# Kernel optimization log

Hardware: AMD Instinct MI355X
Metric: run time of the kernel (lower is better)

The kernel has to match this reference:

```python
import jax, jax.numpy as jnp
import numpy as np

WS = 8  # window size (8,8); num_token n = 64


def setup_inputs() -> dict:
    key = jax.random.key(0)
    ks = jax.random.split(key, 10)
    dim = 28        # channels c
    d = 28          # dim_head
    rank = 28       # sq_dim
    n = WS * WS     # tokens per window
    x = jax.random.normal(ks[0], (1, 8, 256, 256, dim), jnp.float32)

    def lin(k, shape, fan_in):
        return jax.random.normal(k, shape, jnp.float32) / np.sqrt(fan_in).astype(np.float32)

    return {
        "x": x,
        "W_qk": lin(ks[1], (2 * rank, dim), dim),   # to_qk (no bias)
        "W_v": lin(ks[2], (dim, dim), dim),         # to_v (no bias)
        "W_out": lin(ks[3], (dim, dim), dim),       # to_out weight
        "b_out": jnp.zeros((dim,), jnp.float32),    # to_out bias
        "W_pcq": lin(ks[4], (1, d), d),             # pc_proj_q
        "b_pcq": jnp.ones((1,), jnp.float32),       # bias_pc_proj_q (init 1.0)
        "W_pck": lin(ks[5], (1, d), d),             # pc_proj_k
        "b_pck": jnp.ones((1,), jnp.float32),
        "W_m1": lin(ks[6], (1, n), n),              # mlp1: Linear(64,1)
        "W_m2a": lin(ks[7], (n, n), n),             # mlp2: Linear(64,64)
        "W_m2b": lin(ks[8], (1, n), n),             # mlp2: Linear(64,1)
    }


def _fa_forward(x, W_qk, W_v, W_out, b_out, W_pcq, b_pcq, W_pck, b_pck, W_m1, W_m2a, W_m2b):
    b, B, H, Wd, c = x.shape
    nh, nw = H // WS, Wd // WS
    n = WS * WS
    heads = 1  # dim_head == dim == sq_dim -> heads_qk = heads_v = 1
    # window partition: 'b B (h b0) (w b1) c -> (b h w) (b0 b1) B c'
    xw = (x.reshape(b, B, nh, WS, nw, WS, c)
           .transpose(0, 2, 4, 3, 5, 1, 6)
           .reshape(b * nh * nw, n, B, c))
    qk = xw @ W_qk.T                      # [w, n, B, 2*rank]
    q, k = jnp.split(qk, 2, axis=-1)
    v = xw @ W_v.T

    def split_heads(t):                   # [w, n, B, h*d] -> [w, h, B, n, d]
        w_, n_, B_, _ = t.shape
        return t.reshape(w_, n_, B_, heads, -1).transpose(0, 3, 2, 1, 4)

    q, k, v = split_heads(q), split_heads(k), split_heads(v)

    # learned sigma per token
    sig_q = q @ W_pcq.T + b_pcq           # [w, h, B, n, 1]
    sig_k = k @ W_pck.T + b_pck
    sim = jnp.einsum('whBid,whBjd->whBij', q, k)          # raw scores
    Sigma = sig_q * jnp.swapaxes(sig_k, -1, -2)           # outer product [.., i, j]
    # diagonal removal: sim - diag_embed(diag(sim)) == zero the diagonal
    eye = jnp.eye(n, dtype=sim.dtype)
    sim_norm = sim * (1.0 - eye)
    # MLP threshold
    theta = jnp.einsum('whBij,j->whBi', sim_norm, W_m1[0])  # mlp1 over j, squeeze
    t = theta @ W_m2a.T
    t = jnp.where(t >= 0, t, 0.1 * t)                       # LeakyReLU(0.1)
    theta = (t @ W_m2b.T)[..., None]                        # [w, h, B, 1, 1]
    sim = sim * Sigma
    attn = jax.nn.softmax(sim, axis=-1) * (sim > theta).astype(sim.dtype)
    out = jnp.einsum('whBij,whBjd->whBid', attn, v)
    # merge heads: [w, h, B, n, d] -> [w, n, B, h*d]
    out = out.transpose(0, 3, 2, 1, 4).reshape(b * nh * nw, n, B, c)
    out = out @ W_out.T + b_out
    # un-window: '(b h w) (b0 b1) B c -> b B (h b0) (w b1) c'
    out = (out.reshape(b, nh, nw, WS, WS, B, c)
              .transpose(0, 5, 1, 3, 2, 4, 6)
              .reshape(b, B, H, Wd, c))
    return out


def reference(x, W_qk, W_v, W_out, b_out, W_pcq, b_pcq, W_pck, b_pck, W_m1, W_m2a, W_m2b):
    return _fa_forward(x, W_qk, W_v, W_out, b_out, W_pcq, b_pcq,
                       W_pck, b_pck, W_m1, W_m2a, W_m2b)
```

## Files before the change

kernel.cpp:

```cpp
#include <hip/hip_runtime.h>
#include <math.h>

#define C 28
#define N 64

typedef float ff2 __attribute__((ext_vector_type(2)));

#define A_OFF   0
#define QT_OFF  0
#define KT_OFF  1792
#define V_OFF   2048
#define SQ_OFF  3840
#define SGK_OFF 3904
#define TH_OFF  3968
#define LDS_FLOATS 4032

__device__ __forceinline__ float prefix8_asc(float s) {
    float p = s;
    #pragma unroll
    for (int k = 0; k < 7; ++k) {
        int sh = __builtin_amdgcn_update_dpp(0, __float_as_int(p),
                                             0x111 , 0xF, 0xF, true);
        p = __int_as_float(sh) + s;
    }
    return p;
}

__device__ __forceinline__ float max8_dpp(float m) {
    int t;
    t = __builtin_amdgcn_update_dpp(0, __float_as_int(m), 0xB1,  0xF, 0xF, true);
    m = fmaxf(m, __int_as_float(t));
    t = __builtin_amdgcn_update_dpp(0, __float_as_int(m), 0x4E,  0xF, 0xF, true);
    m = fmaxf(m, __int_as_float(t));
    t = __builtin_amdgcn_update_dpp(0, __float_as_int(m), 0x141, 0xF, 0xF, true);
    m = fmaxf(m, __int_as_float(t));
    return m;
}

__global__ __launch_bounds__(128, 8)
void fa_tiled(const float* __restrict__ x,
              const float* __restrict__ Wqk,
              const float* __restrict__ Wv,
              const float* __restrict__ Wout,
              const float* __restrict__ bout,
              const float* __restrict__ Wpcq,
              const float* __restrict__ bpcq,
              const float* __restrict__ Wpck,
              const float* __restrict__ bpck,
              const float* __restrict__ Wm1,
              const float* __restrict__ Wm2a,
              const float* __restrict__ Wm2b,
              float* __restrict__ out)
{
    __shared__ float S[LDS_FLOATS];

    const int tid = threadIdx.x;
    const int wv  = tid >> 6;
    const int ln  = tid & 63;
    const int pid = blockIdx.x;
    const int win = pid >> 3;
    const int Bi  = pid & 7;
    const int hw = win >> 5, ww = win & 31;
    const int b0 = ln >> 3, b1 = ln & 7;
    const size_t base = ((((size_t)Bi * 256) + (size_t)(hw * 8 + b0)) * 256
                         + (size_t)(ww * 8 + b1)) * C;

    const int ti = tid >> 3;
    const int tj = tid & 7;
    const int rg = ti & 7;
    const int gb = ln & 56;

    float vv[16];

    {
        float xr[C];
        {
            const float4* p = (const float4*)(x + base);
            #pragma unroll
            for (int i = 0; i < 7; ++i) {
                float4 t = p[i];
                xr[4*i+0] = t.x; xr[4*i+1] = t.y; xr[4*i+2] = t.z; xr[4*i+3] = t.w;
            }
        }

        if (wv == 0) {
            ff2 sq2 = {0.f, 0.f};
            #pragma unroll 2
            for (int d4 = 0; d4 < 7; ++d4) {
                float qq[4];
                #pragma unroll
                for (int t = 0; t < 4; ++t) {
                    const int d = 4*d4 + t;
                    ff2 a = {0.f, 0.f};
                    #pragma unroll
                    for (int c = 0; c < C; c += 2) {
                        ff2 w = *(const ff2*)&Wqk[d*C + c];
                        ff2 xv; xv.x = xr[c]; xv.y = xr[c+1];
                        a += w * xv;
                    }
                    qq[t] = a.x + a.y;
                    S[QT_OFF + d*64 + ln] = qq[t];
                }
                ff2 q01; q01.x = qq[0]; q01.y = qq[1];
                ff2 q23; q23.x = qq[2]; q23.y = qq[3];
                ff2 w01 = *(const ff2*)&Wpcq[4*d4];
                ff2 w23 = *(const ff2*)&Wpcq[4*d4+2];
                sq2 += q01 * w01;
                sq2 += q23 * w23;
            }
            S[SQ_OFF + ln] = sq2.x + sq2.y + bpcq[0];
            #pragma unroll
            for (int d4 = 0; d4 < 4; ++d4) {
                #pragma unroll
                for (int t = 0; t < 4; ++t) {
                    const int d = 4*d4 + t;
                    ff2 a = {0.f, 0.f};
                    #pragma unroll
                    for (int c = 0; c < C; c += 2) {
                        ff2 w = *(const ff2*)&Wv[d*C + c];
                        ff2 xv; xv.x = xr[c]; xv.y = xr[c+1];
                        a += w * xv;
                    }
                    vv[4*d4+t] = a.x + a.y;
                }
            }
        } else {
            float ak = 0.f;
            #pragma unroll 2
            for (int d4 = 0; d4 < 7; ++d4) {
                float kk[4];
                #pragma unroll
                for (int t = 0; t < 4; ++t) {
                    const int d = 4*d4 + t;
                    ff2 a = {0.f, 0.f};
                    #pragma unroll
                    for (int c = 0; c < C; c += 2) {
                        ff2 w = *(const ff2*)&Wqk[(C+d)*C + c];
                        ff2 xv; xv.x = xr[c]; xv.y = xr[c+1];
                        a += w * xv;
                    }
                    kk[t] = a.x + a.y;
                    S[KT_OFF + d*64 + ln] = kk[t];
                }
                ak += kk[0] * Wpck[4*d4+0];
                ak += kk[1] * Wpck[4*d4+1];
                ak += kk[2] * Wpck[4*d4+2];
                ak += kk[3] * Wpck[4*d4+3];
            }
            S[SGK_OFF + ln] = ak + bpck[0];
            #pragma unroll
            for (int d4 = 4; d4 < 7; ++d4) {
                #pragma unroll
                for (int t = 0; t < 4; ++t) {
                    const int d = 4*d4 + t;
                    ff2 a = {0.f, 0.f};
                    #pragma unroll
                    for (int c = 0; c < C; c += 2) {
                        ff2 w = *(const ff2*)&Wv[d*C + c];
                        ff2 xv; xv.x = xr[c]; xv.y = xr[c+1];
                        a += w * xv;
                    }
                    vv[4*(d4-4)+t] = a.x + a.y;
                }
            }
        }
    }
    __syncthreads();

    ff2 acc2[8][2];
    #pragma unroll
    for (int cc = 0; cc < 8; ++cc) {
        acc2[cc][0] = (ff2){0.f, 0.f};
        acc2[cc][1] = (ff2){0.f, 0.f};
    }

    #pragma unroll 2
    for (int d = 0; d < C; ++d) {
        float4 qa = *(const float4*)&S[QT_OFF + d*64 + 4*ti];
        float4 ka = *(const float4*)&S[KT_OFF + d*64 + 8*tj];
        float4 kb = *(const float4*)&S[KT_OFF + d*64 + 8*tj + 4];
        ff2 q0; q0.x = qa.x; q0.y = qa.y;
        ff2 q1; q1.x = qa.z; q1.y = qa.w;
        float k8[8] = {ka.x,ka.y,ka.z,ka.w,kb.x,kb.y,kb.z,kb.w};
        #pragma unroll
        for (int cc = 0; cc < 8; ++cc) {
            ff2 ks; ks.x = k8[cc]; ks.y = k8[cc];
            acc2[cc][0] += q0 * ks;
            acc2[cc][1] += q1 * ks;
        }
    }

    {
        float4 wa = *(const float4*)&Wm1[8*tj];
        float4 wb = *(const float4*)&Wm1[8*tj + 4];
        float w8[8] = {wa.x,wa.y,wa.z,wa.w,wb.x,wb.y,wb.z,wb.w};
        const bool e0 = (4*ti == 8*tj);
        const bool e4 = (4*ti - 8*tj == 4);
        float th4[4];
        #pragma unroll
        for (int rr = 0; rr < 4; ++rr) {
            float s = 0.f;
            #pragma unroll
            for (int cc = 0; cc < 8; ++cc) {
                float av = acc2[cc][rr >> 1][rr & 1];
                float term = av * w8[cc];
                if (cc == rr     && e0) term = 0.f;
                if (cc == rr + 4 && e4) term = 0.f;
                s += term;
            }
            th4[rr] = prefix8_asc(s);
        }
        if (tj == 7)
            *(float4*)&S[TH_OFF + 4*ti] =
                make_float4(th4[0], th4[1], th4[2], th4[3]);
    }
    __syncthreads();

    if (wv == 0) {
        *(float4*)&S[V_OFF + ln*C +  0] = make_float4(vv[0], vv[1], vv[2], vv[3]);
        *(float4*)&S[V_OFF + ln*C +  4] = make_float4(vv[4], vv[5], vv[6], vv[7]);
        *(float4*)&S[V_OFF + ln*C +  8] = make_float4(vv[8], vv[9], vv[10],vv[11]);
        *(float4*)&S[V_OFF + ln*C + 12] = make_float4(vv[12],vv[13],vv[14],vv[15]);
    } else {
        *(float4*)&S[V_OFF + ln*C + 16] = make_float4(vv[0], vv[1], vv[2], vv[3]);
        *(float4*)&S[V_OFF + ln*C + 20] = make_float4(vv[4], vv[5], vv[6], vv[7]);
        *(float4*)&S[V_OFF + ln*C + 24] = make_float4(vv[8], vv[9], vv[10],vv[11]);
    }

    float theta;
    {
        const float* wrow = Wm2a + ln * N;
        ff2 A = {0.f, 0.f}, B = {0.f, 0.f};
        #pragma unroll 4
        for (int i4 = 0; i4 < 16; ++i4) {
            float4 t4 = *(const float4*)&S[TH_OFF + 4*i4];
            float4 w4 = *(const float4*)&wrow[4*i4];
            ff2 tl; tl.x = t4.x; tl.y = t4.y;
            ff2 th; th.x = t4.z; th.y = t4.w;
            ff2 wl; wl.x = w4.x; wl.y = w4.y;
            ff2 wh; wh.x = w4.z; wh.y = w4.w;
            A += tl * wl;
            B += th * wh;
        }
        float t = (A.x + A.y) + (B.x + B.y);
        t = (t >= 0.f) ? t : 0.1f * t;
        theta = t * Wm2b[ln];
        #pragma unroll
        for (int off = 32; off > 0; off >>= 1)
            theta += __shfl_xor(theta, off, 64);
    }

    {
        float4 a = *(const float4*)&S[SQ_OFF + 4*ti];
        ff2 sq0; sq0.x = a.x; sq0.y = a.y;
        ff2 sq1; sq1.x = a.z; sq1.y = a.w;
        float4 c0 = *(const float4*)&S[SGK_OFF + 8*tj];
        float4 c1 = *(const float4*)&S[SGK_OFF + 8*tj + 4];
        float sg8[8] = {c0.x,c0.y,c0.z,c0.w,c1.x,c1.y,c1.z,c1.w};
        #pragma unroll
        for (int cc = 0; cc < 8; ++cc) {
            ff2 gs; gs.x = sg8[cc]; gs.y = sg8[cc];
            acc2[cc][0] = (acc2[cc][0] * sq0) * gs;
            acc2[cc][1] = (acc2[cc][1] * sq1) * gs;
        }
    }

    float m4[4];
    #pragma unroll
    for (int rr = 0; rr < 4; ++rr) {
        float mp = -1e30f;
        #pragma unroll
        for (int cc = 0; cc < 8; ++cc) mp = fmaxf(mp, acc2[cc][rr >> 1][rr & 1]);
        m4[rr] = max8_dpp(mp);
    }

    float z4[4];
    #pragma unroll
    for (int rr = 0; rr < 4; ++rr) {
        float zp = 0.f;
        #pragma unroll
        for (int cc = 0; cc < 8; ++cc) {
            float ss = acc2[cc][rr >> 1][rr & 1];
            float e = __expf(ss - m4[rr]);
            zp += e;
            acc2[cc][rr >> 1][rr & 1] = (ss > theta) ? e : 0.f;
        }
        float zpre = prefix8_asc(zp);
        z4[rr] = __shfl(zpre, gb + 7, 64);
    }

    float* Aw = &S[A_OFF + 1024*wv];
    if ((tj >> 2) == 0) {
        #pragma unroll
        for (int cc = 0; cc < 8; ++cc) {
            const int jl = 8*(tj & 3) + cc;
            *(float4*)&Aw[jl*32 + ((4*rg + 4*(jl >> 3)) & 31)] =
                make_float4(acc2[cc][0].x, acc2[cc][0].y, acc2[cc][1].x, acc2[cc][1].y);
        }
    }
    __syncthreads();

    const int dg  = tj;
    const int dgc = (dg < 7) ? dg : 6;
    ff2 pv[4][2];
    #pragma unroll
    for (int rr = 0; rr < 4; ++rr) {
        pv[rr][0] = (ff2){0.f, 0.f};
        pv[rr][1] = (ff2){0.f, 0.f};
    }

    #pragma unroll 8
    for (int jl = 0; jl < 32; ++jl) {
        float4 a4 = *(const float4*)&Aw[jl*32 + ((4*rg + 4*(jl >> 3)) & 31)];
        float4 v4 = *(const float4*)&S[V_OFF + jl*C + 4*dgc];
        ff2 vlo; vlo.x = v4.x; vlo.y = v4.y;
        ff2 vhi; vhi.x = v4.z; vhi.y = v4.w;
        float a8[4] = {a4.x, a4.y, a4.z, a4.w};
        #pragma unroll
        for (int rr = 0; rr < 4; ++rr) {
            ff2 as; as.x = a8[rr]; as.y = a8[rr];
            pv[rr][0] += as * vlo;
            pv[rr][1] += as * vhi;
        }
    }

    if ((tj >> 2) == 1) {
        #pragma unroll
        for (int cc = 0; cc < 8; ++cc) {
            const int jl = 8*(tj & 3) + cc;
            *(float4*)&Aw[jl*32 + ((4*rg + 4*(jl >> 3)) & 31)] =
                make_float4(acc2[cc][0].x, acc2[cc][0].y, acc2[cc][1].x, acc2[cc][1].y);
        }
    }

    #pragma unroll 8
    for (int jl = 0; jl < 32; ++jl) {
        float4 a4 = *(const float4*)&Aw[jl*32 + ((4*rg + 4*(jl >> 3)) & 31)];
        float4 v4 = *(const float4*)&S[V_OFF + (32 + jl)*C + 4*dgc];
        ff2 vlo; vlo.x = v4.x; vlo.y = v4.y;
        ff2 vhi; vhi.x = v4.z; vhi.y = v4.w;
        float a8[4] = {a4.x, a4.y, a4.z, a4.w};
        #pragma unroll
        for (int rr = 0; rr < 4; ++rr) {
            ff2 as; as.x = a8[rr]; as.y = a8[rr];
            pv[rr][0] += as * vlo;
            pv[rr][1] += as * vhi;
        }
    }

    #pragma unroll
    for (int rr = 0; rr < 4; ++rr) {
        float rz = 1.0f / z4[rr];
        ff2 rz2; rz2.x = rz; rz2.y = rz;
        pv[rr][0] *= rz2;
        pv[rr][1] *= rz2;
    }

    if (dg < 7) {
        #pragma unroll
        for (int rr = 0; rr < 4; ++rr)
            *(float4*)&Aw[(4*rg+rr)*C + 4*dg] =
                make_float4(pv[rr][0].x, pv[rr][0].y, pv[rr][1].x, pv[rr][1].y);
    }
    __syncthreads();

    float o[C];
    {
        const float* orow = &S[A_OFF + 1024*(ln >> 5) + (ln & 31)*C];
        #pragma unroll
        for (int i = 0; i < 7; ++i) {
            float4 t = *(const float4*)(orow + 4*i);
            o[4*i+0] = t.x; o[4*i+1] = t.y; o[4*i+2] = t.z; o[4*i+3] = t.w;
        }
    }
    if (wv == 0) {
        float y[16];
        #pragma unroll 2
        for (int e4 = 0; e4 < 4; ++e4) {
            #pragma unroll
            for (int t = 0; t < 4; ++t) {
                const int e = 4*e4 + t;
                ff2 a = {0.f, 0.f};
                #pragma unroll
                for (int d = 0; d < C; d += 2) {
                    ff2 w = *(const ff2*)&Wout[e*C + d];
                    ff2 ov; ov.x = o[d]; ov.y = o[d+1];
                    a += w * ov;
                }
                y[e] = (a.x + a.y) + bout[e];
            }
        }
        float4* yp = (float4*)(out + base);
        #pragma unroll
        for (int i = 0; i < 4; ++i)
            yp[i] = make_float4(y[4*i+0], y[4*i+1], y[4*i+2], y[4*i+3]);
    } else {
        float y[12];
        #pragma unroll 2
        for (int e4 = 0; e4 < 3; ++e4) {
            #pragma unroll
            for (int t = 0; t < 4; ++t) {
                const int e = 16 + 4*e4 + t;
                ff2 a = {0.f, 0.f};
                #pragma unroll
                for (int d = 0; d < C; d += 2) {
                    ff2 w = *(const ff2*)&Wout[e*C + d];
                    ff2 ov; ov.x = o[d]; ov.y = o[d+1];
                    a += w * ov;
                }
                y[4*e4+t] = (a.x + a.y) + bout[e];
            }
        }
        float4* yp = (float4*)(out + base + 16);
        #pragma unroll
        for (int i = 0; i < 3; ++i)
            yp[i] = make_float4(y[4*i+0], y[4*i+1], y[4*i+2], y[4*i+3]);
    }
}

extern "C" void kernel_launch(void* const* d_in, const int* in_sizes, int n_in,
                              void* d_out, int out_size, void* d_ws, size_t ws_size,
                              hipStream_t stream) {
    const float* x     = (const float*)d_in[0];
    const float* W_qk  = (const float*)d_in[1];
    const float* W_v   = (const float*)d_in[2];
    const float* W_out = (const float*)d_in[3];
    const float* b_out = (const float*)d_in[4];
    const float* W_pcq = (const float*)d_in[5];
    const float* b_pcq = (const float*)d_in[6];
    const float* W_pck = (const float*)d_in[7];
    const float* b_pck = (const float*)d_in[8];
    const float* W_m1  = (const float*)d_in[9];
    const float* W_m2a = (const float*)d_in[10];
    const float* W_m2b = (const float*)d_in[11];
    float* y = (float*)d_out;

    hipLaunchKernelGGL(fa_tiled, dim3(8192), dim3(128), 0, stream,
                       x, W_qk, W_v, W_out, b_out, W_pcq, b_pcq,
                       W_pck, b_pck, W_m1, W_m2a, W_m2b, y);
}
```

Baseline: 216.8 us.

## Shrink LDS footprint by staging K in halves and quartering attention buffer

Cuts shared memory per block from 4032 to 3008 floats. K is now staged in two passes: the first 16 dims go to LDS while the last 12 stay in registers until the first QK pass finishes. The PV product now streams attention in quarters of 16 columns instead of halves of 32, and the output staging is rearranged so each wave handles its own token half. More resident blocks per CU should improve occupancy, at the cost of extra barriers and more registers held across the QK loop.

```diff
diff --git a/kernel.cpp b/kernel.cpp
--- a/kernel.cpp
+++ b/kernel.cpp
@@ -6,14 +6,15 @@
 
 typedef float ff2 __attribute__((ext_vector_type(2)));
 
+#define QT_OFF  0
+#define KTH_OFF 1792
 #define A_OFF   0
-#define QT_OFF  0
-#define KT_OFF  1792
-#define V_OFF   2048
-#define SQ_OFF  3840
-#define SGK_OFF 3904
-#define TH_OFF  3968
-#define LDS_FLOATS 4032
+#define V_OFF   1024
+#define OT_OFF  0
+#define SQ_OFF  2816
+#define SGK_OFF 2880
+#define TH_OFF  2944
+#define LDS_FLOATS 3008
 
 __device__ __forceinline__ float prefix8_asc(float s) {
     float p = s;
@@ -70,7 +71,7 @@
     const int rg = ti & 7;
     const int gb = ln & 56;
 
-    float vv[16];
+    float st[24];
 
     {
         float xr[C];
@@ -121,13 +122,13 @@
                         ff2 xv; xv.x = xr[c]; xv.y = xr[c+1];
                         a += w * xv;
                     }
-                    vv[4*d4+t] = a.x + a.y;
+                    st[4*d4+t] = a.x + a.y;
                 }
             }
         } else {
             float ak = 0.f;
-            #pragma unroll 2
-            for (int d4 = 0; d4 < 7; ++d4) {
+            #pragma unroll
+            for (int d4 = 0; d4 < 4; ++d4) {
                 float kk[4];
                 #pragma unroll
                 for (int t = 0; t < 4; ++t) {
@@ -140,7 +141,28 @@
                         a += w * xv;
                     }
                     kk[t] = a.x + a.y;
-                    S[KT_OFF + d*64 + ln] = kk[t];
+                    S[KTH_OFF + d*64 + ln] = kk[t];
+                }
+                ak += kk[0] * Wpck[4*d4+0];
+                ak += kk[1] * Wpck[4*d4+1];
+                ak += kk[2] * Wpck[4*d4+2];
+                ak += kk[3] * Wpck[4*d4+3];
+            }
+            #pragma unroll
+            for (int d4 = 4; d4 < 7; ++d4) {
+                float kk[4];
+                #pragma unroll
+                for (int t = 0; t < 4; ++t) {
+                    const int d = 4*d4 + t;
+                    ff2 a = {0.f, 0.f};
+                    #pragma unroll
+                    for (int c = 0; c < C; c += 2) {
+                        ff2 w = *(const ff2*)&Wqk[(C+d)*C + c];
+                        ff2 xv; xv.x = xr[c]; xv.y = xr[c+1];
+                        a += w * xv;
+                    }
+                    kk[t] = a.x + a.y;
+                    st[12 + 4*(d4-4) + t] = kk[t];
                 }
                 ak += kk[0] * Wpck[4*d4+0];
                 ak += kk[1] * Wpck[4*d4+1];
@@ -160,7 +182,7 @@
                         ff2 xv; xv.x = xr[c]; xv.y = xr[c+1];
                         a += w * xv;
                     }
-                    vv[4*(d4-4)+t] = a.x + a.y;
+                    st[4*(d4-4)+t] = a.x + a.y;
                 }
             }
         }
@@ -175,10 +197,34 @@
     }
 
     #pragma unroll 2
-    for (int d = 0; d < C; ++d) {
+    for (int d = 0; d < 16; ++d) {
         float4 qa = *(const float4*)&S[QT_OFF + d*64 + 4*ti];
-        float4 ka = *(const float4*)&S[KT_OFF + d*64 + 8*tj];
-        float4 kb = *(const float4*)&S[KT_OFF + d*64 + 8*tj + 4];
+        float4 ka = *(const float4*)&S[KTH_OFF + d*64 + 8*tj];
+        float4 kb = *(const float4*)&S[KTH_OFF + d*64 + 8*tj + 4];
+        ff2 q0; q0.x = qa.x; q0.y = qa.y;
+        ff2 q1; q1.x = qa.z; q1.y = qa.w;
+        float k8[8] = {ka.x,ka.y,ka.z,ka.w,kb.x,kb.y,kb.z,kb.w};
+        #pragma unroll
+        for (int cc = 0; cc < 8; ++cc) {
+            ff2 ks; ks.x = k8[cc]; ks.y = k8[cc];
+            acc2[cc][0] += q0 * ks;
+            acc2[cc][1] += q1 * ks;
+        }
+    }
+    __syncthreads();
+
+    if (wv == 1) {
+        #pragma unroll
+        for (int dl = 0; dl < 12; ++dl)
+            S[KTH_OFF + dl*64 + ln] = st[12 + dl];
+    }
+    __syncthreads();
+
+    #pragma unroll 2
+    for (int d = 16; d < 28; ++d) {
+        float4 qa = *(const float4*)&S[QT_OFF + d*64 + 4*ti];
+        float4 ka = *(const float4*)&S[KTH_OFF + (d-16)*64 + 8*tj];
+        float4 kb = *(const float4*)&S[KTH_OFF + (d-16)*64 + 8*tj + 4];
         ff2 q0; q0.x = qa.x; q0.y = qa.y;
         ff2 q1; q1.x = qa.z; q1.y = qa.w;
         float k8[8] = {ka.x,ka.y,ka.z,ka.w,kb.x,kb.y,kb.z,kb.w};
@@ -217,14 +263,14 @@
     __syncthreads();
 
     if (wv == 0) {
-        *(float4*)&S[V_OFF + ln*C +  0] = make_float4(vv[0], vv[1], vv[2], vv[3]);
-        *(float4*)&S[V_OFF + ln*C +  4] = make_float4(vv[4], vv[5], vv[6], vv[7]);
-        *(float4*)&S[V_OFF + ln*C +  8] = make_float4(vv[8], vv[9], vv[10],vv[11]);
-        *(float4*)&S[V_OFF + ln*C + 12] = make_float4(vv[12],vv[13],vv[14],vv[15]);
+        *(float4*)&S[V_OFF + ln*C +  0] = make_float4(st[0], st[1], st[2], st[3]);
+        *(float4*)&S[V_OFF + ln*C +  4] = make_float4(st[4], st[5], st[6], st[7]);
+        *(float4*)&S[V_OFF + ln*C +  8] = make_float4(st[8], st[9], st[10],st[11]);
+        *(float4*)&S[V_OFF + ln*C + 12] = make_float4(st[12],st[13],st[14],st[15]);
     } else {
-        *(float4*)&S[V_OFF + ln*C + 16] = make_float4(vv[0], vv[1], vv[2], vv[3]);
-        *(float4*)&S[V_OFF + ln*C + 20] = make_float4(vv[4], vv[5], vv[6], vv[7]);
-        *(float4*)&S[V_OFF + ln*C + 24] = make_float4(vv[8], vv[9], vv[10],vv[11]);
+        *(float4*)&S[V_OFF + ln*C + 16] = make_float4(st[0], st[1], st[2], st[3]);
+        *(float4*)&S[V_OFF + ln*C + 20] = make_float4(st[4], st[5], st[6], st[7]);
+        *(float4*)&S[V_OFF + ln*C + 24] = make_float4(st[8], st[9], st[10],st[11]);
     }
 
     float theta;
@@ -273,7 +319,6 @@
         for (int cc = 0; cc < 8; ++cc) mp = fmaxf(mp, acc2[cc][rr >> 1][rr & 1]);
         m4[rr] = max8_dpp(mp);
     }
-
     float z4[4];
     #pragma unroll
     for (int rr = 0; rr < 4; ++rr) {
@@ -289,12 +334,12 @@
         z4[rr] = __shfl(zpre, gb + 7, 64);
     }
 
-    float* Aw = &S[A_OFF + 1024*wv];
-    if ((tj >> 2) == 0) {
+    float* Aw = &S[A_OFF + 512*wv];
+    if ((tj >> 1) == 0) {
         #pragma unroll
         for (int cc = 0; cc < 8; ++cc) {
-            const int jl = 8*(tj & 3) + cc;
-            *(float4*)&Aw[jl*32 + ((4*rg + 4*(jl >> 3)) & 31)] =
+            const int jq = 8*(tj & 1) + cc;
+            *(float4*)&Aw[jq*32 + ((4*rg + 4*(jq >> 3)) & 31)] =
                 make_float4(acc2[cc][0].x, acc2[cc][0].y, acc2[cc][1].x, acc2[cc][1].y);
         }
     }
@@ -309,42 +354,29 @@
         pv[rr][1] = (ff2){0.f, 0.f};
     }
 
-    #pragma unroll 8
-    for (int jl = 0; jl < 32; ++jl) {
-        float4 a4 = *(const float4*)&Aw[jl*32 + ((4*rg + 4*(jl >> 3)) & 31)];
-        float4 v4 = *(const float4*)&S[V_OFF + jl*C + 4*dgc];
-        ff2 vlo; vlo.x = v4.x; vlo.y = v4.y;
-        ff2 vhi; vhi.x = v4.z; vhi.y = v4.w;
-        float a8[4] = {a4.x, a4.y, a4.z, a4.w};
-        #pragma unroll
-        for (int rr = 0; rr < 4; ++rr) {
-            ff2 as; as.x = a8[rr]; as.y = a8[rr];
-            pv[rr][0] += as * vlo;
-            pv[rr][1] += as * vhi;
-        }
-    }
-
-    if ((tj >> 2) == 1) {
-        #pragma unroll
-        for (int cc = 0; cc < 8; ++cc) {
-            const int jl = 8*(tj & 3) + cc;
-            *(float4*)&Aw[jl*32 + ((4*rg + 4*(jl >> 3)) & 31)] =
-                make_float4(acc2[cc][0].x, acc2[cc][0].y, acc2[cc][1].x, acc2[cc][1].y);
-        }
-    }
-
-    #pragma unroll 8
-    for (int jl = 0; jl < 32; ++jl) {
-        float4 a4 = *(const float4*)&Aw[jl*32 + ((4*rg + 4*(jl >> 3)) & 31)];
-        float4 v4 = *(const float4*)&S[V_OFF + (32 + jl)*C + 4*dgc];
-        ff2 vlo; vlo.x = v4.x; vlo.y = v4.y;
-        ff2 vhi; vhi.x = v4.z; vhi.y = v4.w;
-        float a8[4] = {a4.x, a4.y, a4.z, a4.w};
-        #pragma unroll
-        for (int rr = 0; rr < 4; ++rr) {
-            ff2 as; as.x = a8[rr]; as.y = a8[rr];
-            pv[rr][0] += as * vlo;
-            pv[rr][1] += as * vhi;
+    #pragma unroll
+    for (int q = 0; q < 4; ++q) {
+        #pragma unroll 8
+        for (int jq = 0; jq < 16; ++jq) {
+            float4 a4 = *(const float4*)&Aw[jq*32 + ((4*rg + 4*(jq >> 3)) & 31)];
+            float4 v4 = *(const float4*)&S[V_OFF + (16*q + jq)*C + 4*dgc];
+            ff2 vlo; vlo.x = v4.x; vlo.y = v4.y;
+            ff2 vhi; vhi.x = v4.z; vhi.y = v4.w;
+            float a8[4] = {a4.x, a4.y, a4.z, a4.w};
+            #pragma unroll
+            for (int rr = 0; rr < 4; ++rr) {
+                ff2 as; as.x = a8[rr]; as.y = a8[rr];
+                pv[rr][0] += as * vlo;
+                pv[rr][1] += as * vhi;
+            }
+        }
+        if (q < 3 && (tj >> 1) == q + 1) {
+            #pragma unroll
+            for (int cc = 0; cc < 8; ++cc) {
+                const int jq = 8*(tj & 1) + cc;
+                *(float4*)&Aw[jq*32 + ((4*rg + 4*(jq >> 3)) & 31)] =
+                    make_float4(acc2[cc][0].x, acc2[cc][0].y, acc2[cc][1].x, acc2[cc][1].y);
+            }
         }
     }
 
@@ -355,25 +387,31 @@
         pv[rr][0] *= rz2;
         pv[rr][1] *= rz2;
     }
+    __syncthreads();
 
     if (dg < 7) {
         #pragma unroll
         for (int rr = 0; rr < 4; ++rr)
-            *(float4*)&Aw[(4*rg+rr)*C + 4*dg] =
+            *(float4*)&S[OT_OFF + 896*wv + (4*rg+rr)*C + 4*dg] =
                 make_float4(pv[rr][0].x, pv[rr][0].y, pv[rr][1].x, pv[rr][1].y);
     }
-    __syncthreads();
-
+
+    const int tk  = ln & 31;
+    const int eh  = ln >> 5;
+    const int tok = 32*wv + tk;
+    const int ob0 = tok >> 3, ob1 = tok & 7;
+    const size_t obase = ((((size_t)Bi * 256) + (size_t)(hw * 8 + ob0)) * 256
+                          + (size_t)(ww * 8 + ob1)) * C;
     float o[C];
     {
-        const float* orow = &S[A_OFF + 1024*(ln >> 5) + (ln & 31)*C];
+        const float* orow = &S[OT_OFF + 896*wv + tk*C];
         #pragma unroll
         for (int i = 0; i < 7; ++i) {
             float4 t = *(const float4*)(orow + 4*i);
             o[4*i+0] = t.x; o[4*i+1] = t.y; o[4*i+2] = t.z; o[4*i+3] = t.w;
         }
     }
-    if (wv == 0) {
+    if (eh == 0) {
         float y[16];
         #pragma unroll 2
         for (int e4 = 0; e4 < 4; ++e4) {
@@ -390,7 +428,7 @@
                 y[e] = (a.x + a.y) + bout[e];
             }
         }
-        float4* yp = (float4*)(out + base);
+        float4* yp = (float4*)(out + obase);
         #pragma unroll
         for (int i = 0; i < 4; ++i)
             yp[i] = make_float4(y[4*i+0], y[4*i+1], y[4*i+2], y[4*i+3]);
@@ -411,7 +449,7 @@
                 y[4*e4+t] = (a.x + a.y) + bout[e];
             }
         }
-        float4* yp = (float4*)(out + base + 16);
+        float4* yp = (float4*)(out + obase + 16);
         #pragma unroll
         for (int i = 0; i < 3; ++i)
             yp[i] = make_float4(y[4*i+0], y[4*i+1], y[4*i+2], y[4*i+3]);
```

Measured after the change: 224.7 us. 1.04x slower.
